# Optimization experiments

Hardware: AMD Instinct MI355X
Metric: run time of the kernel (lower is better)

Reference implementation:

```python
import jax, jax.numpy as jnp
import numpy as np

NUM_HEADS = 12

def _attn(q, k, v, scale):
    # q,k,v: [..., L, hd]; softmax attention over L (key axis)
    s = jnp.einsum('...qd,...kd->...qk', q, k) * scale
    a = jax.nn.softmax(s, axis=-1)
    return jnp.einsum('...qk,...kd->...qd', a, v)

def setup_inputs() -> dict:
    key = jax.random.key(0)
    k1, k2, k3 = jax.random.split(key, 3)
    B, N, C, D = 8, 256, 16, 768
    x = jax.random.normal(k1, (B, N, C, D), dtype=jnp.float32)
    w_qkv = jax.random.normal(k2, (D, 6 * D), dtype=jnp.float32) * (D ** -0.5)
    w_proj = jax.random.normal(k3, (D, D), dtype=jnp.float32) * (D ** -0.5)
    b_proj = jnp.zeros((D,), dtype=jnp.float32)
    return {"x": x, "w_qkv": w_qkv, "w_proj": w_proj, "b_proj": b_proj}

def reference(x, w_qkv, w_proj, b_proj):
    B, N, C, D = x.shape
    H = NUM_HEADS
    hd = D // H
    scale = hd ** -0.5
    # qkv: [B,N,C,6,H,hd] -> [6,B,H,N,C,hd]
    qkv = (x @ w_qkv).reshape(B, N, C, 6, H, hd).transpose(3, 0, 4, 1, 2, 5)
    qc, kc, qs, ks, vc, vs = qkv[0], qkv[1], qkv[2], qkv[3], qkv[4], qkv[5]
    # spatial attention over N (per channel c): move to [B,H,C,N,hd]
    qs = jnp.swapaxes(qs, -2, -3)
    ks = jnp.swapaxes(ks, -2, -3)
    vs = jnp.swapaxes(vs, -2, -3)
    xs = _attn(qs, ks, vs, scale)          # [B,H,C,N,hd]
    xs = jnp.swapaxes(xs, -2, -3)          # [B,H,N,C,hd]
    # channel attention over C (per token n)
    xc = _attn(qc, kc, vc, scale)          # [B,H,N,C,hd]
    out = xs * xc                           # elementwise combine (fused path)
    # matches torch: x.transpose(1,2).reshape(B,N,C,D)
    out = out.transpose(0, 2, 1, 3, 4).reshape(B, N, C, D)
    return out @ w_proj + b_proj
```

## Files before the change

kernel.cpp:

```cpp
#include <hip/hip_runtime.h>

typedef _Float16 f16;
typedef f16  f16x8 __attribute__((ext_vector_type(8)));
typedef float f32x4 __attribute__((ext_vector_type(4)));

#define S3 3145728LL

__device__ __forceinline__ f32x4 mm(f16x8 a, f16x8 b, f32x4 c) {
  return __builtin_amdgcn_mfma_f32_16x16x32_f16(a, b, c, 0, 0, 0);
}
__device__ __forceinline__ void BAR() { asm volatile("s_barrier" ::: "memory"); }

__device__ __forceinline__ int esw(int t, int col) {
  return t * 128 + ((((col >> 3) ^ ((t ^ (t >> 3)) & 7)) << 3) | (col & 7));
}
__device__ __forceinline__ int oesw(int t, int col) {
  return t * 64 + ((((col >> 3) ^ (t & 7)) << 3) | (col & 7));
}

__global__ void cvt_T_kernel(const float* __restrict__ in, f16* __restrict__ out,
                             int R, int Cc) {
  __shared__ float tile[32][33];
  int tc = blockIdx.x, tr = blockIdx.y;
  int lr = threadIdx.x & 31, lw = threadIdx.x >> 5;
  int c0 = tc * 32, r0 = tr * 32;
#pragma unroll
  for (int i = 0; i < 4; i++)
    tile[lw + 8 * i][lr] = in[(size_t)(r0 + lw + 8 * i) * Cc + c0 + lr];
  __syncthreads();
#pragma unroll
  for (int i = 0; i < 4; i++)
    out[(size_t)(c0 + lw + 8 * i) * R + r0 + lr] = (f16)tile[lr][lw + 8 * i];
}

__global__ void cvt_x_kernel(const float* __restrict__ in, f16* __restrict__ out) {
  size_t i = ((size_t)blockIdx.x * 256 + threadIdx.x) * 8;
  f32x4 a = __builtin_nontemporal_load((const f32x4*)(in + i));
  f32x4 b = __builtin_nontemporal_load((const f32x4*)(in + i + 4));
  f16x8 o;
#pragma unroll
  for (int j = 0; j < 4; j++) { o[j] = (f16)a[j]; o[4 + j] = (f16)b[j]; }
  *(f16x8*)(out + i) = o;
}

#define QST_A(c, q, kt) __builtin_amdgcn_global_load_lds( \
    (const __attribute__((address_space(1))) void*)(aSrc + (size_t)(q) * 24576 + (size_t)(kt) * 64), \
    (__attribute__((address_space(3))) void*)((char*)lds + (c) * 32768 + (q) * 1024 * 4 + wave * 1024), 16, 0, 0)
#define QST_B(c, q, kt) __builtin_amdgcn_global_load_lds( \
    (const __attribute__((address_space(1))) void*)(bSrc + (size_t)(q) * 24576 + (size_t)(kt) * 64), \
    (__attribute__((address_space(3))) void*)((char*)lds + 16384 + (c) * 32768 + (q) * 1024 * 4 + wave * 1024), 16, 0, 0)

__global__ __launch_bounds__(256, 2) void gemm_qkvT(
    const f16* __restrict__ A, const f16* __restrict__ Bt,
    f16* __restrict__ area, long long cstr_) {
  __shared__ f16 lds[32768];
  size_t cstr = (size_t)cstr_;
  int id  = blockIdx.x;
  int cpx = gridDim.x >> 3;
  int id2 = (id & 7) * cpx + (id >> 3);
  int sr = id2 / 288, rr = id2 % 288;
  int bm = sr * 8 + (rr & 7), bn = rr >> 3;

  int tid = threadIdx.x;
  int wave = tid >> 6, lane = tid & 63;
  int l16 = lane & 15, lq = lane >> 4;
  int wr = wave >> 1, wc = wave & 1;
  int l7 = l16 & 7;
  int cb0 = ((lq) ^ l7) << 4;
  int cb1 = ((4 + lq) ^ l7) << 4;

  const f16* aSrc = A  + (size_t)(bm * 128 + (tid >> 3)) * 768 +
                    (((tid & 7) ^ ((tid >> 3) & 7)) << 3);
  const f16* bSrc = Bt + (size_t)(bn * 128 + (tid >> 3)) * 768 +
                    (((tid & 7) ^ ((tid >> 3) & 7)) << 3);

  f32x4 zz = {0.f, 0.f, 0.f, 0.f};
  f32x4 acc[4][4];
#pragma unroll
  for (int m = 0; m < 4; m++)
#pragma unroll
    for (int n = 0; n < 4; n++) acc[m][n] = zz;

#pragma unroll
  for (int q = 0; q < 4; q++) { QST_A(0, q, 0); }
#pragma unroll
  for (int q = 0; q < 4; q++) { QST_B(0, q, 0); }
#pragma unroll
  for (int q = 0; q < 4; q++) { QST_A(1, q, 1); }
#pragma unroll
  for (int q = 0; q < 4; q++) { QST_B(1, q, 1); }
  asm volatile("s_waitcnt vmcnt(8)" ::: "memory");
  BAR();

  f16x8 af[4][2], bf[4][2];
#pragma unroll 2
  for (int t = 0; t < 12; ++t) {
    int c = t & 1;
    const char* ab = (const char*)lds + c * 32768;
    const char* bb = ab + 16384;
    int rA = wr * 64 + l16;
    int rB = wc * 64 + l16;
#pragma unroll
    for (int mf = 0; mf < 4; mf++) {
      af[mf][0] = *(const f16x8*)(ab + (rA + mf * 16) * 128 + cb0);
      af[mf][1] = *(const f16x8*)(ab + (rA + mf * 16) * 128 + cb1);
    }
#pragma unroll
    for (int nf = 0; nf < 4; nf++) {
      bf[nf][0] = *(const f16x8*)(bb + (rB + nf * 16) * 128 + cb0);
      bf[nf][1] = *(const f16x8*)(bb + (rB + nf * 16) * 128 + cb1);
    }
    asm volatile("s_waitcnt lgkmcnt(0)" ::: "memory");
    BAR();
    if (t < 10) {
#pragma unroll
      for (int q = 0; q < 4; q++) { QST_A(c, q, t + 2); }
#pragma unroll
      for (int q = 0; q < 4; q++) { QST_B(c, q, t + 2); }
    }
    __builtin_amdgcn_s_setprio(1);
#pragma unroll
    for (int ks = 0; ks < 2; ks++)
#pragma unroll
      for (int mf = 0; mf < 4; mf++)
#pragma unroll
        for (int nf = 0; nf < 4; nf++)
          acc[mf][nf] = mm(af[mf][ks], bf[nf][ks], acc[mf][nf]);
    __builtin_amdgcn_s_setprio(0);
    if (t < 10) asm volatile("s_waitcnt vmcnt(8)" ::: "memory");
    else        asm volatile("s_waitcnt vmcnt(0)" ::: "memory");
    BAR();
  }

  int s  = bn / 6;
  int h0 = (bn % 6) * 2;
  size_t comp;
  if (s == 0) comp = 0; else if (s == 1) comp = 1; else if (s == 2) comp = 3;
  else if (s == 3) comp = 4; else if (s == 4) comp = 2; else comp = 5;
  int g = (bm * 128) >> 12;
  size_t base = comp * cstr + (size_t)g * S3;
  int n0 = (bm & 31) * 8;

  __syncthreads();
#pragma unroll
  for (int mi = 0; mi < 4; mi++)
#pragma unroll
    for (int ni = 0; ni < 4; ni++)
#pragma unroll
      for (int r = 0; r < 4; r++) {
        int t = wr * 64 + mi * 16 + lq * 4 + r;
        int col = wc * 64 + ni * 16 + l16;
        lds[esw(t, col)] = (f16)acc[mi][ni][r];
      }
  __syncthreads();

  if (s < 2) {
#pragma unroll
    for (int i = 0; i < 4; i++) {
      int u = wave * 4 + i;
      int hl = u >> 3, j16 = u & 7;
#pragma unroll
      for (int half = 0; half < 2; half++) {
        int e0 = half * 512 + lane * 8;
        int cc = e0 >> 6, d0 = e0 & 63;
        f16x8 v = *(const f16x8*)&lds[esw(j16 * 16 + cc, hl * 64 + d0)];
        __builtin_nontemporal_store(v, (f16x8*)&area[base +
            (size_t)(h0 + hl) * 262144 + (size_t)(n0 + j16) * 1024 + e0]);
      }
    }
  } else if (s < 4) {
#pragma unroll
    for (int i = 0; i < 8; i++) {
      int u = wave * 8 + i;
      int hl = u >> 4, cc = u & 15;
      int e = lane * 8;
      int nl = e >> 6, d0 = e & 63;
      f16x8 v = *(const f16x8*)&lds[esw(nl * 16 + cc, hl * 64 + d0)];
      __builtin_nontemporal_store(v, (f16x8*)&area[base +
          (size_t)((h0 + hl) * 16 + cc) * 16384 + (size_t)n0 * 64 + e]);
    }
  } else if (s == 4) {
#pragma unroll
    for (int i = 0; i < 4; i++) {
      int u = wave * 4 + i;
      int hl = u >> 3, j8 = u & 7;
#pragma unroll
      for (int half = 0; half < 2; half++) {
        int e0 = half * 512 + lane * 8;
        int d0 = e0 >> 4, cb = e0 & 15;
        f16x8 v;
#pragma unroll
        for (int j = 0; j < 8; j++)
          v[j] = lds[esw(j8 * 16 + cb + j, hl * 64 + d0)];
        __builtin_nontemporal_store(v, (f16x8*)&area[base +
            (size_t)((h0 + hl) * 256 + n0 + j8) * 1024 + e0]);
      }
    }
  } else {
#pragma unroll
    for (int i = 0; i < 8; i++) {
      int u = wave * 8 + i;
      int hl = u >> 4, cc = u & 15;
      int e = lane * 8;
      int d0 = e >> 3;
      f16x8 v;
#pragma unroll
      for (int j = 0; j < 8; j++)
        v[j] = lds[esw(j * 16 + cc, hl * 64 + d0)];
      __builtin_nontemporal_store(v, (f16x8*)&area[base +
          ((size_t)((h0 + hl) * 16 + cc) * 32 + (bm & 31)) * 512 + e]);
    }
  }
}

__global__ __launch_bounds__(256, 2) void gemm_projT(
    const f16* __restrict__ A,
    const f16* __restrict__ Bt,
    const float* __restrict__ bias, float* __restrict__ Cout) {
  __shared__ f16 lds[32768];
  int id  = blockIdx.x;
  int cpx = gridDim.x >> 3;
  int id2 = (id & 7) * cpx + (id >> 3);
  int sr = id2 / 48, rr = id2 % 48;
  int bm = sr * 8 + (rr & 7), bn = rr >> 3;

  int tid = threadIdx.x;
  int wave = tid >> 6, lane = tid & 63;
  int l16 = lane & 15, lq = lane >> 4;
  int wr = wave >> 1, wc = wave & 1;
  int l7 = l16 & 7;
  int cb0 = ((lq) ^ l7) << 4;
  int cb1 = ((4 + lq) ^ l7) << 4;

  const f16* aSrc = A  + (size_t)(bm * 128 + (tid >> 3)) * 768 +
                    (((tid & 7) ^ ((tid >> 3) & 7)) << 3);
  const f16* bSrc = Bt + (size_t)(bn * 128 + (tid >> 3)) * 768 +
                    (((tid & 7) ^ ((tid >> 3) & 7)) << 3);

  f32x4 zz = {0.f, 0.f, 0.f, 0.f};
  f32x4 acc[4][4];
#pragma unroll
  for (int m = 0; m < 4; m++)
#pragma unroll
    for (int n = 0; n < 4; n++) acc[m][n] = zz;

#pragma unroll
  for (int q = 0; q < 4; q++) { QST_A(0, q, 0); }
#pragma unroll
  for (int q = 0; q < 4; q++) { QST_B(0, q, 0); }
#pragma unroll
  for (int q = 0; q < 4; q++) { QST_A(1, q, 1); }
#pragma unroll
  for (int q = 0; q < 4; q++) { QST_B(1, q, 1); }
  asm volatile("s_waitcnt vmcnt(8)" ::: "memory");
  BAR();

  f16x8 af[4][2], bf[4][2];
#pragma unroll 2
  for (int t = 0; t < 12; ++t) {
    int c = t & 1;
    const char* ab = (const char*)lds + c * 32768;
    const char* bb = ab + 16384;
    int rA = wr * 64 + l16;
    int rB = wc * 64 + l16;
#pragma unroll
    for (int mf = 0; mf < 4; mf++) {
      af[mf][0] = *(const f16x8*)(ab + (rA + mf * 16) * 128 + cb0);
      af[mf][1] = *(const f16x8*)(ab + (rA + mf * 16) * 128 + cb1);
    }
#pragma unroll
    for (int nf = 0; nf < 4; nf++) {
      bf[nf][0] = *(const f16x8*)(bb + (rB + nf * 16) * 128 + cb0);
      bf[nf][1] = *(const f16x8*)(bb + (rB + nf * 16) * 128 + cb1);
    }
    asm volatile("s_waitcnt lgkmcnt(0)" ::: "memory");
    BAR();
    if (t < 10) {
#pragma unroll
      for (int q = 0; q < 4; q++) { QST_A(c, q, t + 2); }
#pragma unroll
      for (int q = 0; q < 4; q++) { QST_B(c, q, t + 2); }
    }
    __builtin_amdgcn_s_setprio(1);
#pragma unroll
    for (int ks = 0; ks < 2; ks++)
#pragma unroll
      for (int mf = 0; mf < 4; mf++)
#pragma unroll
        for (int nf = 0; nf < 4; nf++)
          acc[mf][nf] = mm(af[mf][ks], bf[nf][ks], acc[mf][nf]);
    __builtin_amdgcn_s_setprio(0);
    if (t < 10) asm volatile("s_waitcnt vmcnt(8)" ::: "memory");
    else        asm volatile("s_waitcnt vmcnt(0)" ::: "memory");
    BAR();
  }

#pragma unroll
  for (int ni = 0; ni < 4; ni++) {
    int col = bn * 128 + wc * 64 + ni * 16 + l16;
    float bb = bias[col];
#pragma unroll
    for (int mi = 0; mi < 4; mi++) {
#pragma unroll
      for (int r = 0; r < 4; r++) {
        int row = bm * 128 + wr * 64 + mi * 16 + lq * 4 + r;
        __builtin_nontemporal_store(acc[mi][ni][r] + bb,
                                    &Cout[(size_t)row * 768 + col]);
      }
    }
  }
}

__global__ __launch_bounds__(256) void attn_chan_kernel(f16* __restrict__ area,
                                                        long long cstr_) {
  size_t cstr = (size_t)cstr_;
  int blk = blockIdx.x;
  int g = blk >> 8, n = blk & 255;
  size_t goff = (size_t)g * S3;
  int tid = threadIdx.x;
  int wave = tid >> 6, lane = tid & 63;
  int l16 = lane & 15, lq = lane >> 4;
  __shared__ f16 prl[12288];
  __shared__ f16 plds[4][16][40];

  if (lane < 16) {
#pragma unroll
    for (int j = 0; j < 16; j++) plds[wave][lane][16 + j] = (f16)0.f;
  }
  __syncthreads();

  f32x4 zz = {0.f, 0.f, 0.f, 0.f};
  for (int hi = 0; hi < 3; hi++) {
    int h = wave + hi * 4;
    const f16* q = area + 0 * cstr + goff + (size_t)((h * 256 + n) * 16) * 64;
    const f16* k = area + 1 * cstr + goff + (size_t)((h * 256 + n) * 16) * 64;
    const f16* v = area + 2 * cstr + goff + (size_t)((h * 256 + n) * 64) * 16;
    f16x8 a0 = *(const f16x8*)&q[l16 * 64 + lq * 8];
    f16x8 a1 = *(const f16x8*)&q[l16 * 64 + 32 + lq * 8];
    f16x8 b0 = *(const f16x8*)&k[l16 * 64 + lq * 8];
    f16x8 b1 = *(const f16x8*)&k[l16 * 64 + 32 + lq * 8];
    f32x4 s = mm(a1, b1, mm(a0, b0, zz));
    float p[4];
#pragma unroll
    for (int r = 0; r < 4; r++) {
      float t = s[r] * 0.125f;
      float mx = t;
      mx = fmaxf(mx, __shfl_xor(mx, 1));
      mx = fmaxf(mx, __shfl_xor(mx, 2));
      mx = fmaxf(mx, __shfl_xor(mx, 4));
      mx = fmaxf(mx, __shfl_xor(mx, 8));
      float e = __expf(t - mx);
      float sum = e;
      sum += __shfl_xor(sum, 1);
      sum += __shfl_xor(sum, 2);
      sum += __shfl_xor(sum, 4);
      sum += __shfl_xor(sum, 8);
      p[r] = e / sum;
    }
#pragma unroll
    for (int r = 0; r < 4; r++)
      plds[wave][lq * 4 + r][l16] = (f16)p[r];
    f16x8 ap = *(const f16x8*)&plds[wave][l16][lq * 8];
#pragma unroll
    for (int nt = 0; nt < 4; nt++) {
      f16x8 bv = *(const f16x8*)&v[(nt * 16 + l16) * 16 + lq * 8];
      f32x4 o = mm(ap, bv, zz);
#pragma unroll
      for (int r = 0; r < 4; r++) {
        int cq = lq * 4 + r, d = nt * 16 + l16;
        prl[h * 1024 + cq * 64 + d] = (f16)o[r];
      }
    }
  }
  __syncthreads();
  f16* xc = area + 6 * cstr + goff + (size_t)n * 12288;
#pragma unroll
  for (int i = 0; i < 6; i++) {
    f16x8 v = *(const f16x8*)&prl[i * 2048 + tid * 8];
    __builtin_nontemporal_store(v, (f16x8*)&xc[i * 2048 + tid * 8]);
  }
}

__global__ __launch_bounds__(512) void attn_spat_kernel(f16* __restrict__ area,
                                                        long long cstr_) {
  size_t cstr = (size_t)cstr_;
  int blk = blockIdx.x;
  int g = blk / 192, rem = blk % 192;
  int h = rem >> 4, c = rem & 15;
  size_t goff = (size_t)g * S3;
  const f16* qs = area + 3 * cstr + goff + (size_t)((h * 16 + c) * 256) * 64;
  const f16* ks = area + 4 * cstr + goff + (size_t)((h * 16 + c) * 256) * 64;
  const f16* vsb = area + 5 * cstr + goff + (size_t)(h * 16 + c) * 16384;
  f16* xcn = area + 6 * cstr + goff;

  int tid = threadIdx.x;
  int wave = tid >> 6, lane = tid & 63;
  int l16 = lane & 15, lq = lane >> 4;
  __shared__ f16 plds[8][32][40];
  __shared__ f16 osm[16384];

  f32x4 zz = {0.f, 0.f, 0.f, 0.f};
  f16x8 aq[2][2];
#pragma unroll
  for (int m = 0; m < 2; m++)
#pragma unroll
    for (int kd = 0; kd < 2; kd++)
      aq[m][kd] = *(const f16x8*)&qs[(size_t)(wave * 32 + m * 16 + l16) * 64 + kd * 32 + lq * 8];

  f32x4 o[2][4];
  float mrow[2][4], lrow[2][4];
#pragma unroll
  for (int m = 0; m < 2; m++) {
#pragma unroll
    for (int n = 0; n < 4; n++) o[m][n] = zz;
#pragma unroll
    for (int r = 0; r < 4; r++) { mrow[m][r] = -1e30f; lrow[m][r] = 0.f; }
  }

  for (int kc = 0; kc < 8; kc++) {
    int k0 = kc * 32;
    f16x8 bk00 = *(const f16x8*)&ks[(size_t)(k0 + l16) * 64 + lq * 8];
    f16x8 bk01 = *(const f16x8*)&ks[(size_t)(k0 + l16) * 64 + 32 + lq * 8];
    f16x8 bk10 = *(const f16x8*)&ks[(size_t)(k0 + 16 + l16) * 64 + lq * 8];
    f16x8 bk11 = *(const f16x8*)&ks[(size_t)(k0 + 16 + l16) * 64 + 32 + lq * 8];
    f32x4 st[2][2];
#pragma unroll
    for (int m = 0; m < 2; m++) {
      st[m][0] = mm(aq[m][1], bk01, mm(aq[m][0], bk00, zz));
      st[m][1] = mm(aq[m][1], bk11, mm(aq[m][0], bk10, zz));
    }
#pragma unroll
    for (int m = 0; m < 2; m++) {
#pragma unroll
      for (int r = 0; r < 4; r++) {
        float s0 = st[m][0][r] * 0.125f, s1 = st[m][1][r] * 0.125f;
        float t = fmaxf(s0, s1);
        t = fmaxf(t, __shfl_xor(t, 1));
        t = fmaxf(t, __shfl_xor(t, 2));
        t = fmaxf(t, __shfl_xor(t, 4));
        t = fmaxf(t, __shfl_xor(t, 8));
        float mold = mrow[m][r];
        if (!__all(t - mold <= 8.f)) {
          float mnew = fmaxf(mold, t);
          float fac  = __expf(mold - mnew);
          mrow[m][r] = mnew;
          lrow[m][r] *= fac;
          o[m][0][r] *= fac; o[m][1][r] *= fac; o[m][2][r] *= fac; o[m][3][r] *= fac;
          mold = mnew;
        }
        float p0 = __expf(s0 - mold), p1 = __expf(s1 - mold);
        lrow[m][r] += p0 + p1;
        int prow = m * 16 + lq * 4 + r;
        plds[wave][prow][l16]      = (f16)p0;
        plds[wave][prow][16 + l16] = (f16)p1;
      }
    }
    f16x8 ap0 = *(const f16x8*)&plds[wave][l16][lq * 8];
    f16x8 ap1 = *(const f16x8*)&plds[wave][16 + l16][lq * 8];
#pragma unroll
    for (int n = 0; n < 4; n++) {
      f16x8 bv = *(const f16x8*)&vsb[((k0 >> 3) + lq) * 512 + (n * 16 + l16) * 8];
      o[0][n] = mm(ap0, bv, o[0][n]);
      o[1][n] = mm(ap1, bv, o[1][n]);
    }
  }
#pragma unroll
  for (int m = 0; m < 2; m++)
#pragma unroll
    for (int r = 0; r < 4; r++) {
      float l = lrow[m][r];
      l += __shfl_xor(l, 1);
      l += __shfl_xor(l, 2);
      l += __shfl_xor(l, 4);
      l += __shfl_xor(l, 8);
      lrow[m][r] = 1.0f / l;
    }
#pragma unroll
  for (int m = 0; m < 2; m++)
#pragma unroll
    for (int n = 0; n < 4; n++)
#pragma unroll
      for (int r = 0; r < 4; r++) {
        int row = wave * 32 + m * 16 + lq * 4 + r;
        osm[oesw(row, n * 16 + l16)] = (f16)(o[m][n][r] * lrow[m][r]);
      }
  __syncthreads();
  size_t hc64 = (size_t)(h * 16 + c) * 64;
#pragma unroll
  for (int i = 0; i < 4; i++) {
    int row = i * 64 + (tid >> 3);
    int dp  = (tid & 7) * 8;
    size_t dst = (size_t)row * 12288 + hc64 + dp;
    f16x8 v   = *(const f16x8*)&osm[oesw(row, dp)];
    f16x8 xcv = *(const f16x8*)&xcn[dst];
    f16x8 pv;
#pragma unroll
    for (int j = 0; j < 8; j++)
      pv[j] = (f16)((float)v[j] * (float)xcv[j]);
    __builtin_nontemporal_store(pv, (f16x8*)&xcn[dst]);
  }
}

extern "C" void kernel_launch(void* const* d_in, const int* in_sizes, int n_in,
                              void* d_out, int out_size, void* d_ws, size_t ws_size,
                              hipStream_t stream) {
  const float* x      = (const float*)d_in[0];
  const float* w_qkv  = (const float*)d_in[1];
  const float* w_proj = (const float*)d_in[2];
  const float* b_proj = (const float*)d_in[3];
  float* out = (float*)d_out;
  f16* ws = (f16*)d_ws;

  const size_t W16T = 4608ull * 768;
  const size_t WPT  = 768ull * 768;
  f16* w16t = ws;
  f16* wpt  = ws + W16T;
  f16* area = wpt + WPT;

  int G = 8;
  while (G > 1 && (W16T + WPT + 7ull * G * S3) * 2 > ws_size) G >>= 1;
  int nch = 8 / G;
  long long cstr = (long long)G * S3;
  f16* x16 = area + 6 * (size_t)cstr;

  cvt_T_kernel<<<dim3(144, 24), 256, 0, stream>>>(w_qkv, w16t, 768, 4608);
  cvt_T_kernel<<<dim3(24, 24), 256, 0, stream>>>(w_proj, wpt, 768, 768);

  for (int ch = 0; ch < nch; ch++) {
    size_t b0 = (size_t)ch * G;
    cvt_x_kernel<<<G * 1536, 256, 0, stream>>>(x + b0 * S3, x16);
    gemm_qkvT<<<G * 1152, 256, 0, stream>>>(x16, w16t, area, cstr);
    attn_chan_kernel<<<G * 256, 256, 0, stream>>>(area, cstr);
    attn_spat_kernel<<<G * 192, 512, 0, stream>>>(area, cstr);
    gemm_projT<<<G * 192, 256, 0, stream>>>(area + 6 * (size_t)cstr, wpt, b_proj,
                                            out + b0 * S3);
  }
}
```

Baseline: 484.3 us.

## Halve GEMM K-tile to 32 and shrink LDS for four blocks per CU

Both the QKV and projection GEMMs now use a K-step of 32 instead of 64. Each double-buffered LDS stage shrinks to 16 KB, the XOR swizzle is rebuilt for 64-byte rows, and the shared loop is factored into macros. Launch bounds rise from 2 to 4 blocks per CU, aiming for higher occupancy and better latency hiding. The cost is twice as many loop iterations and barriers per tile, with less MFMA work between each synchronization.

```diff
diff --git a/kernel.cpp b/kernel.cpp
--- a/kernel.cpp
+++ b/kernel.cpp
@@ -43,17 +43,62 @@
   *(f16x8*)(out + i) = o;
 }
 
-#define QST_A(c, q, kt) __builtin_amdgcn_global_load_lds( \
-    (const __attribute__((address_space(1))) void*)(aSrc + (size_t)(q) * 24576 + (size_t)(kt) * 64), \
-    (__attribute__((address_space(3))) void*)((char*)lds + (c) * 32768 + (q) * 1024 * 4 + wave * 1024), 16, 0, 0)
-#define QST_B(c, q, kt) __builtin_amdgcn_global_load_lds( \
-    (const __attribute__((address_space(1))) void*)(bSrc + (size_t)(q) * 24576 + (size_t)(kt) * 64), \
-    (__attribute__((address_space(3))) void*)((char*)lds + 16384 + (c) * 32768 + (q) * 1024 * 4 + wave * 1024), 16, 0, 0)
-
-__global__ __launch_bounds__(256, 2) void gemm_qkvT(
+#define Q3_A(c, kt) do { \
+    __builtin_amdgcn_global_load_lds( \
+      (const __attribute__((address_space(1))) void*)(aSrc + (size_t)(kt) * 32), \
+      (__attribute__((address_space(3))) void*)((char*)lds + (c) * 16384 + (tid >> 2) * 64 + (tid & 3) * 16), 16, 0, 0); \
+    __builtin_amdgcn_global_load_lds( \
+      (const __attribute__((address_space(1))) void*)(aSrc + 49152 + (size_t)(kt) * 32), \
+      (__attribute__((address_space(3))) void*)((char*)lds + (c) * 16384 + 4096 + (tid >> 2) * 64 + (tid & 3) * 16), 16, 0, 0); \
+  } while (0)
+#define Q3_B(c, kt) do { \
+    __builtin_amdgcn_global_load_lds( \
+      (const __attribute__((address_space(1))) void*)(bSrc + (size_t)(kt) * 32), \
+      (__attribute__((address_space(3))) void*)((char*)lds + (c) * 16384 + 8192 + (tid >> 2) * 64 + (tid & 3) * 16), 16, 0, 0); \
+    __builtin_amdgcn_global_load_lds( \
+      (const __attribute__((address_space(1))) void*)(bSrc + 49152 + (size_t)(kt) * 32), \
+      (__attribute__((address_space(3))) void*)((char*)lds + (c) * 16384 + 12288 + (tid >> 2) * 64 + (tid & 3) * 16), 16, 0, 0); \
+  } while (0)
+
+#define GEMM32_LOOP()                                                          \
+  f16x8 af[4], bf[4];                                                          \
+  _Pragma("unroll 2")                                                          \
+  for (int t = 0; t < 24; ++t) {                                               \
+    int c = t & 1;                                                             \
+    const char* ab = (const char*)lds + c * 16384;                             \
+    const char* bb = ab + 8192;                                                \
+    int rA = wr * 64 + l16;                                                    \
+    int rB = wc * 64 + l16;                                                    \
+    _Pragma("unroll")                                                          \
+    for (int mf = 0; mf < 4; mf++)                                             \
+      af[mf] = *(const f16x8*)(ab + (rA + mf * 16) * 64 + cb);                 \
+    _Pragma("unroll")                                                          \
+    for (int nf = 0; nf < 4; nf++)                                             \
+      bf[nf] = *(const f16x8*)(bb + (rB + nf * 16) * 64 + cb);                 \
+    asm volatile("s_waitcnt lgkmcnt(0)" ::: "memory");                         \
+    BAR();                                                                     \
+    if (t < 22) { Q3_A(c, t + 2); Q3_B(c, t + 2); }                            \
+    __builtin_amdgcn_s_setprio(1);                                             \
+    _Pragma("unroll")                                                          \
+    for (int mf = 0; mf < 4; mf++)                                             \
+      _Pragma("unroll")                                                        \
+      for (int nf = 0; nf < 4; nf++)                                           \
+        acc[mf][nf] = mm(af[mf], bf[nf], acc[mf][nf]);                         \
+    __builtin_amdgcn_s_setprio(0);                                             \
+    if (t < 22) asm volatile("s_waitcnt vmcnt(4)" ::: "memory");               \
+    else        asm volatile("s_waitcnt vmcnt(0)" ::: "memory");               \
+    BAR();                                                                     \
+  }
+
+#define GEMM32_PROLOGUE()                                                      \
+  Q3_A(0, 0); Q3_B(0, 0); Q3_A(1, 1); Q3_B(1, 1);                              \
+  asm volatile("s_waitcnt vmcnt(4)" ::: "memory");                             \
+  BAR();
+
+__global__ __launch_bounds__(256, 4) void gemm_qkvT(
     const f16* __restrict__ A, const f16* __restrict__ Bt,
     f16* __restrict__ area, long long cstr_) {
-  __shared__ f16 lds[32768];
+  __shared__ f16 lds[16384];
   size_t cstr = (size_t)cstr_;
   int id  = blockIdx.x;
   int cpx = gridDim.x >> 3;
@@ -65,14 +110,12 @@
   int wave = tid >> 6, lane = tid & 63;
   int l16 = lane & 15, lq = lane >> 4;
   int wr = wave >> 1, wc = wave & 1;
-  int l7 = l16 & 7;
-  int cb0 = ((lq) ^ l7) << 4;
-  int cb1 = ((4 + lq) ^ l7) << 4;
-
-  const f16* aSrc = A  + (size_t)(bm * 128 + (tid >> 3)) * 768 +
-                    (((tid & 7) ^ ((tid >> 3) & 7)) << 3);
-  const f16* bSrc = Bt + (size_t)(bn * 128 + (tid >> 3)) * 768 +
-                    (((tid & 7) ^ ((tid >> 3) & 7)) << 3);
+  int cb = ((lq ^ (l16 & 3)) << 4);
+
+  const f16* aSrc = A  + (size_t)(bm * 128 + (tid >> 2)) * 768 +
+                    (((tid & 3) ^ ((tid >> 2) & 3)) << 3);
+  const f16* bSrc = Bt + (size_t)(bn * 128 + (tid >> 2)) * 768 +
+                    (((tid & 3) ^ ((tid >> 2) & 3)) << 3);
 
   f32x4 zz = {0.f, 0.f, 0.f, 0.f};
   f32x4 acc[4][4];
@@ -81,56 +124,8 @@
 #pragma unroll
     for (int n = 0; n < 4; n++) acc[m][n] = zz;
 
-#pragma unroll
-  for (int q = 0; q < 4; q++) { QST_A(0, q, 0); }
-#pragma unroll
-  for (int q = 0; q < 4; q++) { QST_B(0, q, 0); }
-#pragma unroll
-  for (int q = 0; q < 4; q++) { QST_A(1, q, 1); }
-#pragma unroll
-  for (int q = 0; q < 4; q++) { QST_B(1, q, 1); }
-  asm volatile("s_waitcnt vmcnt(8)" ::: "memory");
-  BAR();
-
-  f16x8 af[4][2], bf[4][2];
-#pragma unroll 2
-  for (int t = 0; t < 12; ++t) {
-    int c = t & 1;
-    const char* ab = (const char*)lds + c * 32768;
-    const char* bb = ab + 16384;
-    int rA = wr * 64 + l16;
-    int rB = wc * 64 + l16;
-#pragma unroll
-    for (int mf = 0; mf < 4; mf++) {
-      af[mf][0] = *(const f16x8*)(ab + (rA + mf * 16) * 128 + cb0);
-      af[mf][1] = *(const f16x8*)(ab + (rA + mf * 16) * 128 + cb1);
-    }
-#pragma unroll
-    for (int nf = 0; nf < 4; nf++) {
-      bf[nf][0] = *(const f16x8*)(bb + (rB + nf * 16) * 128 + cb0);
-      bf[nf][1] = *(const f16x8*)(bb + (rB + nf * 16) * 128 + cb1);
-    }
-    asm volatile("s_waitcnt lgkmcnt(0)" ::: "memory");
-    BAR();
-    if (t < 10) {
-#pragma unroll
-      for (int q = 0; q < 4; q++) { QST_A(c, q, t + 2); }
-#pragma unroll
-      for (int q = 0; q < 4; q++) { QST_B(c, q, t + 2); }
-    }
-    __builtin_amdgcn_s_setprio(1);
-#pragma unroll
-    for (int ks = 0; ks < 2; ks++)
-#pragma unroll
-      for (int mf = 0; mf < 4; mf++)
-#pragma unroll
-        for (int nf = 0; nf < 4; nf++)
-          acc[mf][nf] = mm(af[mf][ks], bf[nf][ks], acc[mf][nf]);
-    __builtin_amdgcn_s_setprio(0);
-    if (t < 10) asm volatile("s_waitcnt vmcnt(8)" ::: "memory");
-    else        asm volatile("s_waitcnt vmcnt(0)" ::: "memory");
-    BAR();
-  }
+  GEMM32_PROLOGUE();
+  GEMM32_LOOP();
 
   int s  = bn / 6;
   int h0 = (bn % 6) * 2;
@@ -187,11 +182,11 @@
 #pragma unroll
       for (int half = 0; half < 2; half++) {
         int e0 = half * 512 + lane * 8;
-        int d0 = e0 >> 4, cb = e0 & 15;
+        int d0 = e0 >> 4, cb2 = e0 & 15;
         f16x8 v;
 #pragma unroll
         for (int j = 0; j < 8; j++)
-          v[j] = lds[esw(j8 * 16 + cb + j, hl * 64 + d0)];
+          v[j] = lds[esw(j8 * 16 + cb2 + j, hl * 64 + d0)];
         __builtin_nontemporal_store(v, (f16x8*)&area[base +
             (size_t)((h0 + hl) * 256 + n0 + j8) * 1024 + e0]);
       }
@@ -213,11 +208,11 @@
   }
 }
 
-__global__ __launch_bounds__(256, 2) void gemm_projT(
+__global__ __launch_bounds__(256, 4) void gemm_projT(
     const f16* __restrict__ A,
     const f16* __restrict__ Bt,
     const float* __restrict__ bias, float* __restrict__ Cout) {
-  __shared__ f16 lds[32768];
+  __shared__ f16 lds[16384];
   int id  = blockIdx.x;
   int cpx = gridDim.x >> 3;
   int id2 = (id & 7) * cpx + (id >> 3);
@@ -228,14 +223,12 @@
   int wave = tid >> 6, lane = tid & 63;
   int l16 = lane & 15, lq = lane >> 4;
   int wr = wave >> 1, wc = wave & 1;
-  int l7 = l16 & 7;
-  int cb0 = ((lq) ^ l7) << 4;
-  int cb1 = ((4 + lq) ^ l7) << 4;
-
-  const f16* aSrc = A  + (size_t)(bm * 128 + (tid >> 3)) * 768 +
-                    (((tid & 7) ^ ((tid >> 3) & 7)) << 3);
-  const f16* bSrc = Bt + (size_t)(bn * 128 + (tid >> 3)) * 768 +
-                    (((tid & 7) ^ ((tid >> 3) & 7)) << 3);
+  int cb = ((lq ^ (l16 & 3)) << 4);
+
+  const f16* aSrc = A  + (size_t)(bm * 128 + (tid >> 2)) * 768 +
+                    (((tid & 3) ^ ((tid >> 2) & 3)) << 3);
+  const f16* bSrc = Bt + (size_t)(bn * 128 + (tid >> 2)) * 768 +
+                    (((tid & 3) ^ ((tid >> 2) & 3)) << 3);
 
   f32x4 zz = {0.f, 0.f, 0.f, 0.f};
   f32x4 acc[4][4];
@@ -244,56 +237,8 @@
 #pragma unroll
     for (int n = 0; n < 4; n++) acc[m][n] = zz;
 
-#pragma unroll
-  for (int q = 0; q < 4; q++) { QST_A(0, q, 0); }
-#pragma unroll
-  for (int q = 0; q < 4; q++) { QST_B(0, q, 0); }
-#pragma unroll
-  for (int q = 0; q < 4; q++) { QST_A(1, q, 1); }
-#pragma unroll
-  for (int q = 0; q < 4; q++) { QST_B(1, q, 1); }
-  asm volatile("s_waitcnt vmcnt(8)" ::: "memory");
-  BAR();
-
-  f16x8 af[4][2], bf[4][2];
-#pragma unroll 2
-  for (int t = 0; t < 12; ++t) {
-    int c = t & 1;
-    const char* ab = (const char*)lds + c * 32768;
-    const char* bb = ab + 16384;
-    int rA = wr * 64 + l16;
-    int rB = wc * 64 + l16;
-#pragma unroll
-    for (int mf = 0; mf < 4; mf++) {
-      af[mf][0] = *(const f16x8*)(ab + (rA + mf * 16) * 128 + cb0);
-      af[mf][1] = *(const f16x8*)(ab + (rA + mf * 16) * 128 + cb1);
-    }
-#pragma unroll
-    for (int nf = 0; nf < 4; nf++) {
-      bf[nf][0] = *(const f16x8*)(bb + (rB + nf * 16) * 128 + cb0);
-      bf[nf][1] = *(const f16x8*)(bb + (rB + nf * 16) * 128 + cb1);
-    }
-    asm volatile("s_waitcnt lgkmcnt(0)" ::: "memory");
-    BAR();
-    if (t < 10) {
-#pragma unroll
-      for (int q = 0; q < 4; q++) { QST_A(c, q, t + 2); }
-#pragma unroll
-      for (int q = 0; q < 4; q++) { QST_B(c, q, t + 2); }
-    }
-    __builtin_amdgcn_s_setprio(1);
-#pragma unroll
-    for (int ks = 0; ks < 2; ks++)
-#pragma unroll
-      for (int mf = 0; mf < 4; mf++)
-#pragma unroll
-        for (int nf = 0; nf < 4; nf++)
-          acc[mf][nf] = mm(af[mf][ks], bf[nf][ks], acc[mf][nf]);
-    __builtin_amdgcn_s_setprio(0);
-    if (t < 10) asm volatile("s_waitcnt vmcnt(8)" ::: "memory");
-    else        asm volatile("s_waitcnt vmcnt(0)" ::: "memory");
-    BAR();
-  }
+  GEMM32_PROLOGUE();
+  GEMM32_LOOP();
 
 #pragma unroll
   for (int ni = 0; ni < 4; ni++) {
```

Result: slower. 525.7 us (+8.6%).
